# Optimization experiments

Measured on AMD Instinct MI355X. Metric: run time of the kernel, lower is better.

Reference implementation:

```python
import jax, jax.numpy as jnp
import numpy as np

NHEAD = 8
ATT_EPS = 1e-6
LN_EPS = 1e-5


def _layernorm(x, g, b):
    mu = jnp.mean(x, axis=-1, keepdims=True)
    var = jnp.mean(jnp.square(x - mu), axis=-1, keepdims=True)
    return (x - mu) * jax.lax.rsqrt(var + LN_EPS) * g + b


def setup_inputs() -> dict:
    key = jax.random.key(0)
    ks = jax.random.split(key, 7)
    N, L, C = 4, 16384, 256
    s = 1.0 / np.sqrt(C)
    return {
        "x": jax.random.normal(ks[0], (N, L, C), jnp.float32),
        "Wq": jax.random.normal(ks[1], (C, C), jnp.float32) * s,
        "Wk": jax.random.normal(ks[2], (C, C), jnp.float32) * s,
        "Wv": jax.random.normal(ks[3], (C, C), jnp.float32) * s,
        "Wm": jax.random.normal(ks[4], (C, C), jnp.float32) * s,
        "W1": jax.random.normal(ks[5], (2 * C, 2 * C), jnp.float32) * (1.0 / np.sqrt(2 * C)),
        "W2": jax.random.normal(ks[6], (2 * C, C), jnp.float32) * (1.0 / np.sqrt(2 * C)),
        "g1": jnp.ones((C,), jnp.float32),
        "b1": jnp.zeros((C,), jnp.float32),
        "g2": jnp.ones((C,), jnp.float32),
        "b2": jnp.zeros((C,), jnp.float32),
    }


def reference(x, Wq, Wk, Wv, Wm, W1, W2, g1, b1, g2, b2):
    N, L, C = x.shape
    H = NHEAD
    D = C // H
    # projections -> [N, L, H, D]
    q = (x @ Wq).reshape(N, L, H, D)
    k = (x @ Wk).reshape(N, L, H, D)
    v = (x @ Wv).reshape(N, L, H, D)
    # elu+1 feature map (linear attention)
    Q = jax.nn.elu(q) + 1.0
    K = jax.nn.elu(k) + 1.0
    v = v / L  # values / v_length
    # KV: [N, H, D, Dv]
    KV = jnp.einsum('nshd,nshv->nhdv', K, v)
    # normalizer Z: [N, L, H]
    Z = 1.0 / (jnp.einsum('nlhd,nhd->nlh', Q, K.sum(axis=1)) + ATT_EPS)
    # queried values, rescaled by v_length
    msg = jnp.einsum('nlhd,nhdv,nlh->nlhv', Q, KV, Z) * L  # [N, L, H, Dv]
    # merge heads + norm1
    msg = msg.reshape(N, L, C) @ Wm
    msg = _layernorm(msg, g1, b1)
    # MLP on concat([x, msg]) + norm2
    h = jnp.concatenate([x, msg], axis=-1) @ W1
    h = jax.nn.relu(h) @ W2
    msg = _layernorm(h, g2, b2)
    return x + msg
```

## Files before the change

### kernel.cpp

```cpp
#include <hip/hip_runtime.h>
#include <hip/hip_bf16.h>
#include <math.h>

#define L_SEQ   16384
#define C_DIM   256
#define N_BATCH 4
#define N_HEAD  8
#define D_H     32
#define M_ROWS  (N_BATCH * L_SEQ)
#define KV_SPLIT 64
#define SLAB_E  ((size_t)M_ROWS * C_DIM)

typedef unsigned short u16;
typedef unsigned int   u32;
typedef short s16x8 __attribute__((ext_vector_type(8)));
typedef float f32x4 __attribute__((ext_vector_type(4)));

__device__ __forceinline__ float bf2f(u32 lo16) { return __uint_as_float(lo16 << 16); }
__device__ __forceinline__ u16 f2bf(float f) {
    u32 u = __float_as_uint(f);
    u32 rb = ((u >> 16) & 1u) + 0x7fffu;
    return (u16)((u + rb) >> 16);
}

__device__ __forceinline__ void gl_lds16(const u16* g, u16* l) {
    __builtin_amdgcn_global_load_lds(
        (__attribute__((address_space(1))) void*)g,
        (__attribute__((address_space(3))) void*)l, 16, 0, 0);
}

__global__ __launch_bounds__(256)
void f32_to_bf16_k(const float* __restrict__ in, u16* __restrict__ out, int n8)
{
    int i = blockIdx.x * blockDim.x + threadIdx.x;
    int stride = gridDim.x * blockDim.x;
    for (; i < n8; i += stride) {
        float4 f0 = ((const float4*)in)[(size_t)i * 2];
        float4 f1 = ((const float4*)in)[(size_t)i * 2 + 1];
        uint4 o;
        o.x = (u32)f2bf(f0.x) | ((u32)f2bf(f0.y) << 16);
        o.y = (u32)f2bf(f0.z) | ((u32)f2bf(f0.w) << 16);
        o.z = (u32)f2bf(f1.x) | ((u32)f2bf(f1.y) << 16);
        o.w = (u32)f2bf(f1.z) | ((u32)f2bf(f1.w) << 16);
        ((uint4*)out)[i] = o;
    }
}

__global__ __launch_bounds__(256)
void w_prep(const float* __restrict__ Wq, const float* __restrict__ Wk,
            const float* __restrict__ Wv, const float* __restrict__ Wm,
            const float* __restrict__ W1, const float* __restrict__ W2,
            u16* __restrict__ wqkvt, u16* __restrict__ wmt,
            u16* __restrict__ w1t, u16* __restrict__ w2t)
{
    __shared__ float tile[32][33];
    int bt = blockIdx.x;
    const float* src; u16* dst; int K, N, rowoff, tt;
    if (bt < 192)      { int w = bt >> 6; tt = bt & 63;
                         src = (w == 0) ? Wq : (w == 1) ? Wk : Wv;
                         dst = wqkvt; K = 256; N = 256; rowoff = w * 256; }
    else if (bt < 256) { tt = bt - 192; src = Wm; dst = wmt; K = 256; N = 256; rowoff = 0; }
    else if (bt < 512) { tt = bt - 256; src = W1; dst = w1t; K = 512; N = 512; rowoff = 0; }
    else               { tt = bt - 512; src = W2; dst = w2t; K = 512; N = 256; rowoff = 0; }
    int ntx = N >> 5;
    int n0 = (tt % ntx) * 32, k0 = (tt / ntx) * 32;
    int tx = threadIdx.x & 31, ty = threadIdx.x >> 5;
    #pragma unroll
    for (int i = 0; i < 32; i += 8)
        tile[ty + i][tx] = src[(size_t)(k0 + ty + i) * N + n0 + tx];
    __syncthreads();
    #pragma unroll
    for (int i = 0; i < 32; i += 8)
        dst[(size_t)(rowoff + n0 + ty + i) * K + k0 + tx] = f2bf(tile[tx][ty + i]);
}

template<int EPI>
__global__ __launch_bounds__(256)
void gemm_bf16(const u16* __restrict__ A1, const u16* __restrict__ A2,
               int KA, int sA1, int sA2,
               const u16* __restrict__ Bt, int ldb, int bstride,
               u16* __restrict__ C, int ldc, int K, float escale, int nx)
{
    __shared__ __align__(16) u16 As[2][128 * 32];
    __shared__ __align__(16) u16 Bs[2][128 * 32];

    const int tid = threadIdx.x;
    const int nwg = gridDim.x;
    const int cpx = nwg >> 3;
    const int hb  = blockIdx.x;
    const int lb  = (hb & 7) * cpx + (hb >> 3);
    const int m0 = (lb / nx) * 128;
    const int n0 = (lb % nx) * 128;
    const int w = tid >> 6, lane = tid & 63;
    const int wr = w >> 1, wc = w & 1;
    const int g = lane >> 4, r = lane & 15;

    Bt += (size_t)(m0 / L_SEQ) * bstride;

    f32x4 acc[4][4] = {};

    auto stage = [&](int buf, int kt) {
        #pragma unroll
        for (int i = 0; i < 2; ++i) {
            int li  = i * 256 + tid;
            int row = li >> 2, kc = li & 3;
            int kg = kt * 32 + kc * 8;
            const u16* Ap = (kg < KA) ? A1 : A2;
            int stride    = (kg < KA) ? sA1 : sA2;
            int col       = (kg < KA) ? kg  : kg - KA;
            gl_lds16(Ap + (size_t)(m0 + row) * stride + col, &As[buf][li * 8]);
            gl_lds16(Bt + (size_t)(n0 + row) * ldb + kt * 32 + kc * 8, &Bs[buf][li * 8]);
        }
    };

    const int ktiles = K / 32;
    stage(0, 0);
    __syncthreads();
    int cur = 0;
    for (int kt = 0; kt < ktiles; ++kt) {
        if (kt + 1 < ktiles) stage(cur ^ 1, kt + 1);

        s16x8 a[4], b[4];
        #pragma unroll
        for (int mi = 0; mi < 4; ++mi)
            a[mi] = *(const s16x8*)&As[cur][(wr * 64 + mi * 16 + r) * 32 + g * 8];
        #pragma unroll
        for (int ni = 0; ni < 4; ++ni)
            b[ni] = *(const s16x8*)&Bs[cur][(wc * 64 + ni * 16 + r) * 32 + g * 8];
        #pragma unroll
        for (int mi = 0; mi < 4; ++mi)
            #pragma unroll
            for (int ni = 0; ni < 4; ++ni)
                asm volatile("v_mfma_f32_16x16x32_bf16 %0, %1, %2, %0"
                             : "+v"(acc[mi][ni]) : "v"(b[ni]), "v"(a[mi]));

        __syncthreads();
        cur ^= 1;
    }

    asm volatile("s_nop 7");
    asm volatile("s_nop 7");
    asm volatile("s_nop 7");

    #pragma unroll
    for (int mi = 0; mi < 4; ++mi) {
        int row = m0 + wr * 64 + mi * 16 + r;
        #pragma unroll
        for (int ni = 0; ni < 4; ++ni) {
            int col0 = n0 + wc * 64 + ni * 16 + g * 4;
            ushort4 o;
            #pragma unroll
            for (int j = 0; j < 4; ++j) {
                float v = acc[mi][ni][j];
                if (EPI == 3)      v = (v > 0.f) ? v : 0.f;
                else if (EPI == 4) v = (col0 < 512) ? ((v > 0.f) ? (v + 1.f) : __expf(v))
                                                    : v * escale;
                (&o.x)[j] = f2bf(v);
            }
            if (EPI == 4) {
                u16* dst = (col0 < 256) ? C + (size_t)row * 256 + col0
                         : (col0 < 512) ? C + SLAB_E + (size_t)row * 256 + (col0 - 256)
                                        : C + 2 * SLAB_E + (size_t)row * 256 + (col0 - 512);
                *(ushort4*)dst = o;
            } else {
                *(ushort4*)&C[(size_t)row * ldc + col0] = o;
            }
        }
    }
}

__global__ __launch_bounds__(256)
void kv_partial(const u16* __restrict__ Kf, const u16* __restrict__ Vf, int ld,
                float* __restrict__ part)
{
    int b  = blockIdx.x;
    int s  = b & (KV_SPLIT - 1);
    int nh = b / KV_SPLIT;
    int h  = nh & (N_HEAD - 1);
    int n  = nh / N_HEAD;
    int t  = threadIdx.x;

    __shared__ __align__(16) float Ks[16][D_H];
    __shared__ __align__(16) float Vs[16][D_H];

    const int d   = t >> 3;
    const int dv0 = (t & 7) * 4;
    const int lr  = t >> 4;
    const int lc  = (t & 15) * 2;
    const size_t base = ((size_t)n * L_SEQ) * ld + h * D_H;

    float a0 = 0, a1 = 0, a2 = 0, a3 = 0, asum = 0;
    const int CH = L_SEQ / KV_SPLIT;
    for (int l = s * CH; l < s * CH + CH; l += 16) {
        __syncthreads();
        u32 ku = *(const u32*)&Kf[base + (size_t)(l + lr) * ld + lc];
        u32 vu = *(const u32*)&Vf[base + (size_t)(l + lr) * ld + lc];
        Ks[lr][lc] = bf2f(ku & 0xffff); Ks[lr][lc + 1] = bf2f(ku >> 16);
        Vs[lr][lc] = bf2f(vu & 0xffff); Vs[lr][lc + 1] = bf2f(vu >> 16);
        __syncthreads();
        #pragma unroll
        for (int i = 0; i < 16; ++i) {
            float kv = Ks[i][d];
            float4 vv = *(const float4*)&Vs[i][dv0];
            a0 = fmaf(kv, vv.x, a0);
            a1 = fmaf(kv, vv.y, a1);
            a2 = fmaf(kv, vv.z, a2);
            a3 = fmaf(kv, vv.w, a3);
            asum += kv;
        }
    }
    float* p = part + (size_t)b * 1056;
    p[d * D_H + dv0 + 0] = a0;
    p[d * D_H + dv0 + 1] = a1;
    p[d * D_H + dv0 + 2] = a2;
    p[d * D_H + dv0 + 3] = a3;
    if ((t & 7) == 0) p[1024 + d] = asum;
}

__global__ __launch_bounds__(256)
void kv_final(const float* __restrict__ part, float* __restrict__ KV,
              float* __restrict__ Ksum)
{
    int nh = blockIdx.x;
    int t  = threadIdx.x;
    float ax = 0, ay = 0, az = 0, aw = 0, ssum = 0;
    const float* p0 = part + (size_t)nh * KV_SPLIT * 1056;
    for (int s = 0; s < KV_SPLIT; ++s) {
        const float* p = p0 + (size_t)s * 1056;
        float4 v = *(const float4*)&p[t * 4];
        ax += v.x; ay += v.y; az += v.z; aw += v.w;
        if (t < D_H) ssum += p[1024 + t];
    }
    float4 o = make_float4(ax, ay, az, aw);
    *(float4*)&KV[(size_t)nh * 1024 + t * 4] = o;
    if (t < D_H) Ksum[nh * D_H + t] = ssum;
}

__global__ __launch_bounds__(256)
void bdr_build(const float* __restrict__ KV, u16* __restrict__ bdr)
{
    int idx = blockIdx.x * 256 + threadIdx.x;
    int b = idx >> 16;
    int n = (idx >> 8) & 255;
    int k = idx & 255;
    float v = ((n >> 5) == (k >> 5))
            ? KV[(((size_t)b * N_HEAD + (n >> 5)) * D_H + (n & 31)) * D_H + (k & 31)]
            : 0.f;
    bdr[idx] = f2bf(v);
}

#define NT_TOK 32
__global__ __launch_bounds__(256)
void attn_z(u16* __restrict__ q, const float* __restrict__ Ksum)
{
    const int t = threadIdx.x;
    const int w = t >> 6, lane = t & 63;
    const int tok0 = blockIdx.x * NT_TOK;
    const int n = tok0 / L_SEQ;
    float4 ks = *(const float4*)&Ksum[n * C_DIM + lane * 4];

    for (int i = 0; i < NT_TOK; i += 4) {
        int tok = tok0 + i + w;
        u16* qp = q + (size_t)tok * C_DIM + lane * 4;
        uint2 qu = *(const uint2*)qp;
        float q0 = bf2f(qu.x & 0xffff), q1 = bf2f(qu.x >> 16);
        float q2 = bf2f(qu.y & 0xffff), q3 = bf2f(qu.y >> 16);
        float p = q0 * ks.x + q1 * ks.y + q2 * ks.z + q3 * ks.w;
        p += __shfl_xor(p, 1);
        p += __shfl_xor(p, 2);
        p += __shfl_xor(p, 4);
        float z = (float)L_SEQ / (p + 1e-6f);
        uint2 o;
        o.x = (u32)f2bf(q0 * z) | ((u32)f2bf(q1 * z) << 16);
        o.y = (u32)f2bf(q2 * z) | ((u32)f2bf(q3 * z) << 16);
        *(uint2*)qp = o;
    }
}

template<bool FINAL>
__global__ __launch_bounds__(256)
void ln_rows_bf(const u16* __restrict__ X, const float* __restrict__ g,
                const float* __restrict__ b, const float* __restrict__ xres,
                void* __restrict__ Y)
{
    int row  = blockIdx.x * 4 + (threadIdx.x >> 6);
    int lane = threadIdx.x & 63;
    uint2 u = *(const uint2*)(X + (size_t)row * C_DIM + lane * 4);
    float v0 = bf2f(u.x & 0xffff), v1 = bf2f(u.x >> 16);
    float v2 = bf2f(u.y & 0xffff), v3 = bf2f(u.y >> 16);
    float s  = v0 + v1 + v2 + v3;
    float s2 = v0 * v0 + v1 * v1 + v2 * v2 + v3 * v3;
    #pragma unroll
    for (int off = 1; off < 64; off <<= 1) {
        s  += __shfl_xor(s, off);
        s2 += __shfl_xor(s2, off);
    }
    float mu  = s * (1.0f / C_DIM);
    float var = s2 * (1.0f / C_DIM) - mu * mu;
    float rstd = rsqrtf(var + 1e-5f);
    float4 gv = *(const float4*)&g[lane * 4];
    float4 bv = *(const float4*)&b[lane * 4];
    float o0 = (v0 - mu) * rstd * gv.x + bv.x;
    float o1 = (v1 - mu) * rstd * gv.y + bv.y;
    float o2 = (v2 - mu) * rstd * gv.z + bv.z;
    float o3 = (v3 - mu) * rstd * gv.w + bv.w;
    if (FINAL) {
        float4 xv = *(const float4*)&xres[(size_t)row * C_DIM + lane * 4];
        float4 o = make_float4(o0 + xv.x, o1 + xv.y, o2 + xv.z, o3 + xv.w);
        *(float4*)((float*)Y + (size_t)row * C_DIM + lane * 4) = o;
    } else {
        uint2 o;
        o.x = (u32)f2bf(o0) | ((u32)f2bf(o1) << 16);
        o.y = (u32)f2bf(o2) | ((u32)f2bf(o3) << 16);
        *(uint2*)((u16*)Y + (size_t)row * C_DIM + lane * 4) = o;
    }
}

extern "C" void kernel_launch(void* const* d_in, const int* in_sizes, int n_in,
                              void* d_out, int out_size, void* d_ws, size_t ws_size,
                              hipStream_t stream)
{
    const float* x  = (const float*)d_in[0];
    const float* Wq = (const float*)d_in[1];
    const float* Wk = (const float*)d_in[2];
    const float* Wv = (const float*)d_in[3];
    const float* Wm = (const float*)d_in[4];
    const float* W1 = (const float*)d_in[5];
    const float* W2 = (const float*)d_in[6];
    const float* g1 = (const float*)d_in[7];
    const float* b1 = (const float*)d_in[8];
    const float* g2 = (const float*)d_in[9];
    const float* b2 = (const float*)d_in[10];
    float* out = (float*)d_out;

    u16* xb = (u16*)d_ws;
    u16* q  = xb + SLAB_E;
    u16* k  = q + SLAB_E;
    u16* v  = k + SLAB_E;
    u16* e  = v + SLAB_E;
    u16* ln1 = v;
    u16* m1  = e;
    u16* h   = q;
    u16* mlp = e;
    u16* wqkvt = e + SLAB_E;
    u16* wmt   = wqkvt + 768 * 256;
    u16* w1t   = wmt + 256 * 256;
    u16* w2t   = w1t + 512 * 512;
    u16* bdr   = w2t + 256 * 512;
    u16* bdwt  = bdr + (size_t)N_BATCH * 256 * 256;
    float* KV   = (float*)(bdwt + (size_t)N_BATCH * 256 * 256);
    float* Ksum = KV + (size_t)N_BATCH * N_HEAD * D_H * D_H;
    float* part = Ksum + (size_t)N_BATCH * N_HEAD * D_H;

    dim3 blk(256);
    const float invL = 1.0f / (float)L_SEQ;

    f32_to_bf16_k<<<2048, blk, 0, stream>>>(x, xb, (int)(SLAB_E / 8));
    w_prep<<<640, blk, 0, stream>>>(Wq, Wk, Wv, Wm, W1, W2, wqkvt, wmt, w1t, w2t);

    gemm_bf16<4><<<(M_ROWS / 128) * 6, blk, 0, stream>>>(
        xb, xb, 256, 256, 256, wqkvt, 256, 0, q, 256, 256, invL, 6);

    kv_partial<<<N_BATCH * N_HEAD * KV_SPLIT, blk, 0, stream>>>(k, v, 256, part);
    kv_final<<<N_BATCH * N_HEAD, blk, 0, stream>>>(part, KV, Ksum);

    bdr_build<<<(N_BATCH * 256 * 256) / 256, blk, 0, stream>>>(KV, bdr);
    gemm_bf16<0><<<16, blk, 0, stream>>>(
        wmt, wmt, 256, 256, 256, bdr, 256, 0, bdwt, 1024, 256, 1.f, 8);

    attn_z<<<M_ROWS / NT_TOK, blk, 0, stream>>>(q, Ksum);

    gemm_bf16<0><<<(M_ROWS / 128) * 2, blk, 0, stream>>>(
        q, q, 256, 256, 256, bdwt, 1024, 256, m1, 256, 256, 1.f, 2);
    ln_rows_bf<false><<<M_ROWS / 4, blk, 0, stream>>>(m1, g1, b1, nullptr, (void*)ln1);

    gemm_bf16<3><<<(M_ROWS / 128) * 4, blk, 0, stream>>>(
        xb, ln1, 256, 256, 256, w1t, 512, 0, h, 512, 512, 1.f, 4);
    gemm_bf16<0><<<(M_ROWS / 128) * 2, blk, 0, stream>>>(
        h, h, 512, 512, 512, w2t, 512, 0, mlp, 256, 512, 1.f, 2);

    ln_rows_bf<true><<<M_ROWS / 4, blk, 0, stream>>>(mlp, g2, b2, x, out);
}
```

Measured before the change: 287.5 us.

## Deepen GEMM pipeline to 4 LDS stages with XOR swizzle; widen KV partial tiles

Changes the bf16 GEMM from double buffering to a 4-buffer ring that prefetches two k-tiles ahead. Each iteration waits with explicit vmcnt counts and a single barrier instead of two __syncthreads. It also XOR-swizzles the LDS k-chunk layout to reduce bank conflicts and raises wave priority around the MFMA block. Separately, kv_partial now loads 32 rows per iteration with 8-byte loads, halving its barrier count. The larger LDS footprint (64KB per block) may lower occupancy, and the hand-tuned vmcnt values depend on how many loads each stage issues.

```diff
diff --git a/kernel.cpp b/kernel.cpp
--- a/kernel.cpp
+++ b/kernel.cpp
@@ -81,8 +81,8 @@
                const u16* __restrict__ Bt, int ldb, int bstride,
                u16* __restrict__ C, int ldc, int K, float escale, int nx)
 {
-    __shared__ __align__(16) u16 As[2][128 * 32];
-    __shared__ __align__(16) u16 Bs[2][128 * 32];
+    __shared__ __align__(16) u16 As[4][128 * 32];
+    __shared__ __align__(16) u16 Bs[4][128 * 32];
 
     const int tid = threadIdx.x;
     const int nwg = gridDim.x;
@@ -99,43 +99,51 @@
 
     f32x4 acc[4][4] = {};
 
-    auto stage = [&](int buf, int kt) {
+    auto stage = [&](int st) {
+        int buf = st & 3;
         #pragma unroll
         for (int i = 0; i < 2; ++i) {
             int li  = i * 256 + tid;
             int row = li >> 2, kc = li & 3;
-            int kg = kt * 32 + kc * 8;
+            int kcg = kc ^ ((row >> 1) & 3);
+            int kg = st * 32 + kcg * 8;
             const u16* Ap = (kg < KA) ? A1 : A2;
             int stride    = (kg < KA) ? sA1 : sA2;
             int col       = (kg < KA) ? kg  : kg - KA;
             gl_lds16(Ap + (size_t)(m0 + row) * stride + col, &As[buf][li * 8]);
-            gl_lds16(Bt + (size_t)(n0 + row) * ldb + kt * 32 + kc * 8, &Bs[buf][li * 8]);
+            gl_lds16(Bt + (size_t)(n0 + row) * ldb + st * 32 + kcg * 8,
+                     &Bs[buf][li * 8]);
         }
     };
 
     const int ktiles = K / 32;
-    stage(0, 0);
-    __syncthreads();
-    int cur = 0;
-    for (int kt = 0; kt < ktiles; ++kt) {
-        if (kt + 1 < ktiles) stage(cur ^ 1, kt + 1);
-
+    stage(0);
+    stage(1);
+    const int gs = g ^ ((r >> 1) & 3);
+    for (int s = 0; s < ktiles; ++s) {
+        if (s + 2 < ktiles) stage(s + 2);
+        int rem = ktiles - 1 - s;
+        if (rem >= 2)      asm volatile("s_waitcnt vmcnt(8)" ::: "memory");
+        else if (rem == 1) asm volatile("s_waitcnt vmcnt(4)" ::: "memory");
+        else               asm volatile("s_waitcnt vmcnt(0)" ::: "memory");
+        __builtin_amdgcn_s_barrier();
+
+        const int buf = s & 3;
         s16x8 a[4], b[4];
         #pragma unroll
         for (int mi = 0; mi < 4; ++mi)
-            a[mi] = *(const s16x8*)&As[cur][(wr * 64 + mi * 16 + r) * 32 + g * 8];
+            a[mi] = *(const s16x8*)&As[buf][(wr * 64 + mi * 16 + r) * 32 + gs * 8];
         #pragma unroll
         for (int ni = 0; ni < 4; ++ni)
-            b[ni] = *(const s16x8*)&Bs[cur][(wc * 64 + ni * 16 + r) * 32 + g * 8];
+            b[ni] = *(const s16x8*)&Bs[buf][(wc * 64 + ni * 16 + r) * 32 + gs * 8];
+        __builtin_amdgcn_s_setprio(1);
         #pragma unroll
         for (int mi = 0; mi < 4; ++mi)
             #pragma unroll
             for (int ni = 0; ni < 4; ++ni)
                 asm volatile("v_mfma_f32_16x16x32_bf16 %0, %1, %2, %0"
                              : "+v"(acc[mi][ni]) : "v"(b[ni]), "v"(a[mi]));
-
-        __syncthreads();
-        cur ^= 1;
+        __builtin_amdgcn_s_setprio(0);
     }
 
     asm volatile("s_nop 7");
@@ -180,26 +188,28 @@
     int n  = nh / N_HEAD;
     int t  = threadIdx.x;
 
-    __shared__ __align__(16) float Ks[16][D_H];
-    __shared__ __align__(16) float Vs[16][D_H];
+    __shared__ __align__(16) float Ks[32][D_H];
+    __shared__ __align__(16) float Vs[32][D_H];
 
     const int d   = t >> 3;
     const int dv0 = (t & 7) * 4;
-    const int lr  = t >> 4;
-    const int lc  = (t & 15) * 2;
+    const int lr  = t >> 3;
+    const int lc  = (t & 7) * 4;
     const size_t base = ((size_t)n * L_SEQ) * ld + h * D_H;
 
     float a0 = 0, a1 = 0, a2 = 0, a3 = 0, asum = 0;
     const int CH = L_SEQ / KV_SPLIT;
-    for (int l = s * CH; l < s * CH + CH; l += 16) {
+    for (int l = s * CH; l < s * CH + CH; l += 32) {
         __syncthreads();
-        u32 ku = *(const u32*)&Kf[base + (size_t)(l + lr) * ld + lc];
-        u32 vu = *(const u32*)&Vf[base + (size_t)(l + lr) * ld + lc];
-        Ks[lr][lc] = bf2f(ku & 0xffff); Ks[lr][lc + 1] = bf2f(ku >> 16);
-        Vs[lr][lc] = bf2f(vu & 0xffff); Vs[lr][lc + 1] = bf2f(vu >> 16);
+        uint2 ku = *(const uint2*)&Kf[base + (size_t)(l + lr) * ld + lc];
+        uint2 vu = *(const uint2*)&Vf[base + (size_t)(l + lr) * ld + lc];
+        Ks[lr][lc] = bf2f(ku.x & 0xffff); Ks[lr][lc + 1] = bf2f(ku.x >> 16);
+        Ks[lr][lc + 2] = bf2f(ku.y & 0xffff); Ks[lr][lc + 3] = bf2f(ku.y >> 16);
+        Vs[lr][lc] = bf2f(vu.x & 0xffff); Vs[lr][lc + 1] = bf2f(vu.x >> 16);
+        Vs[lr][lc + 2] = bf2f(vu.y & 0xffff); Vs[lr][lc + 3] = bf2f(vu.y >> 16);
         __syncthreads();
         #pragma unroll
-        for (int i = 0; i < 16; ++i) {
+        for (int i = 0; i < 32; ++i) {
             float kv = Ks[i][d];
             float4 vv = *(const float4*)&Vs[i][dv0];
             a0 = fmaf(kv, vv.x, a0);
```

Result: slower. 305.5 us (+6.3%).
